# Optimization experiments

Measured on AMD Instinct MI355X. Metric: run time of the kernel, lower is better.

Reference implementation:

```python
import jax, jax.numpy as jnp
import numpy as np

B, M, K, E, V, HOPS = 256, 128, 4, 512, 32000, 3


def setup_inputs() -> dict:
    key = jax.random.key(0)
    ks = jax.random.split(key, 12)

    def emb_table(k):
        t = 0.1 * jax.random.normal(k, (V, E), dtype=jnp.float32)
        return t.at[0].set(0.0)  # padding_idx=0

    inp = {
        "context": jax.random.randint(ks[0], (B, M, K), 0, V),
        "y_": jax.random.randint(ks[1], (B,), 0, V),
        "h_": jax.random.normal(ks[2], (1, B, E), dtype=jnp.float32),
        # embedding tables; C[i] tied to A[i+1], so distinct: A0,A1,A2,C2
        "A0": emb_table(ks[3]),
        "A1": emb_table(ks[4]),
        "A2": emb_table(ks[5]),
        "C2": emb_table(ks[6]),
        # GRU (single layer, single step): PyTorch layout [3E, E] and [3E]
        "W_ih": 0.05 * jax.random.normal(ks[7], (3 * E, E), dtype=jnp.float32),
        "W_hh": 0.05 * jax.random.normal(ks[8], (3 * E, E), dtype=jnp.float32),
        "b_ih": jnp.zeros((3 * E,), dtype=jnp.float32),
        "b_hh": jnp.zeros((3 * E,), dtype=jnp.float32),
        # lin_vocab: Linear(2E -> V)
        "lin_W": 0.02 * jax.random.normal(ks[9], (V, 2 * E), dtype=jnp.float32),
        "lin_b": jnp.zeros((V,), dtype=jnp.float32),
    }
    return inp


def _gru_step(x, h, W_ih, W_hh, b_ih, b_hh):
    gi = x @ W_ih.T + b_ih  # [B, 3E]
    gh = h @ W_hh.T + b_hh
    i_r, i_z, i_n = jnp.split(gi, 3, axis=-1)
    h_r, h_z, h_n = jnp.split(gh, 3, axis=-1)
    r = jax.nn.sigmoid(i_r + h_r)
    z = jax.nn.sigmoid(i_z + h_z)
    n = jnp.tanh(i_n + r * h_n)
    return (1.0 - z) * n + z * h


def reference(context, y_, h_, A0, A1, A2, C2, W_ih, W_hh, b_ih, b_hh, lin_W, lin_b):
    # memories[hop] = sum_k A[hop][context], memories[hops] = sum_k C[hops-1][context]
    tables = [A0, A1, A2, C2]
    memories = [t[context].sum(axis=2) for t in tables]  # each [B, M, E]

    m = A1[y_]  # C[0](y_) -- C[0].weight tied to A[1].weight, [B, E]
    h = _gru_step(m, h_[0], W_ih, W_hh, b_ih, b_hh)  # [B, E]

    q = h
    p = None
    p_vocab = None
    for hop in range(HOPS):
        p = jnp.einsum("bme,be->bm", memories[hop], q)  # dot-attention scores
        attn = jax.nn.softmax(p, axis=1)
        o = jnp.einsum("bm,bme->be", attn, memories[hop + 1])
        if hop == 0:
            p_vocab = jnp.concatenate([q, o], axis=1) @ lin_W.T + lin_b  # [B, V]
        q = q + o

    p_ptr = p  # last hop's pre-softmax scores [B, M]
    return (p_ptr, p_vocab, h[None])  # h: [1, B, E]
```

## Files before the change

### kernel.cpp

```cpp
#include <hip/hip_runtime.h>
#include <hip/hip_bf16.h>
#include <stdint.h>
#include <stddef.h>

#define Bb 256
#define Mm 128
#define Ee 512
#define Vv 32000
#define E3 1536

typedef __attribute__((ext_vector_type(8))) short bf16x8;
typedef __attribute__((ext_vector_type(4))) float f32x4;

__device__ __forceinline__ float bf2f(unsigned short u) {
  union { unsigned int i; float f; } v; v.i = ((unsigned int)u) << 16; return v.f;
}
__device__ __forceinline__ unsigned int f2bf(float f) {
  union { float f; unsigned int u; } v; v.f = f;
  unsigned int u = v.u;
  return ((u + 0x7fffu + ((u >> 16) & 1u)) >> 16);
}

#define IN2F_IDX(bb, col)                                                     \
  ((((size_t)((bb) >> 4) * 32 + ((col) >> 5)) * 512) +                        \
   (size_t)((((bb) & 15) + (((col) >> 3) & 3) * 16) * 8 + ((col) & 7)))

__global__ void convert_kernel(const float* __restrict__ A0, const float* __restrict__ A1,
                               const float* __restrict__ A2,
                               unsigned short* __restrict__ tabB) {
  const int t = blockIdx.y;
  const float* src = (t == 0) ? A0 : (t == 1) ? A1 : A2;
  unsigned short* dst = tabB + (size_t)t * Vv * Ee;
  const int n4 = Vv * Ee / 4;
  for (int i = blockIdx.x * blockDim.x + threadIdx.x; i < n4; i += gridDim.x * blockDim.x) {
    f32x4 v = __builtin_nontemporal_load((const f32x4*)src + i);
    unsigned int o0 = f2bf(v.x) | (f2bf(v.y) << 16);
    unsigned int o1 = f2bf(v.z) | (f2bf(v.w) << 16);
    ((uint2*)dst)[i] = make_uint2(o0, o1);
  }
}

__global__ void gru_gemm_kernel(const int* __restrict__ y,
                                const float* __restrict__ A1,
                                const float* __restrict__ hprev,
                                const float* __restrict__ W_ih,
                                const float* __restrict__ W_hh,
                                float* __restrict__ gi,
                                float* __restrict__ gh) {
  const int z = blockIdx.z;
  const float* W = z ? W_hh : W_ih;
  float* C = z ? gh : gi;
  const int by = blockIdx.x * 64;
  const int jy = blockIdx.y * 64;
  __shared__ float As[16][65];
  __shared__ float Bs[16][65];
  const int tx = threadIdx.x & 15, ty = threadIdx.x >> 4;
  float acc[4][4] = {};
  for (int k0 = 0; k0 < Ee; k0 += 16) {
#pragma unroll
    for (int it = 0; it < 4; ++it) {
      int r = ty + it * 16;
      int row = by + r;
      const float* arow = z ? (hprev + (size_t)row * Ee) : (A1 + (size_t)y[row] * Ee);
      As[tx][r] = arow[k0 + tx];
      Bs[tx][r] = W[(size_t)(jy + r) * Ee + k0 + tx];
    }
    __syncthreads();
#pragma unroll
    for (int kk = 0; kk < 16; ++kk) {
      float a[4], bb[4];
#pragma unroll
      for (int i = 0; i < 4; ++i) { a[i] = As[kk][ty * 4 + i]; bb[i] = Bs[kk][tx * 4 + i]; }
#pragma unroll
      for (int i = 0; i < 4; ++i)
#pragma unroll
        for (int j = 0; j < 4; ++j)
          acc[i][j] += a[i] * bb[j];
    }
    __syncthreads();
  }
#pragma unroll
  for (int i = 0; i < 4; ++i)
#pragma unroll
    for (int j = 0; j < 4; ++j)
      C[(size_t)(by + ty * 4 + i) * E3 + jy + tx * 4 + j] = acc[i][j];
}

__global__ __launch_bounds__(1024) void fused_kernel(
    const int* __restrict__ ctx,
    const unsigned short* __restrict__ tabB,
    const float* __restrict__ A0, const float* __restrict__ A1,
    const float* __restrict__ A2,
    const float* __restrict__ gi, const float* __restrict__ gh,
    const float* __restrict__ b_ih, const float* __restrict__ b_hh,
    const float* __restrict__ h0,
    float* __restrict__ out_h, unsigned short* __restrict__ in2f,
    float* __restrict__ p_out) {
  extern __shared__ char smem[];
  unsigned short* Vlds = (unsigned short*)smem;
  float* p_lds = (float*)(smem + 131072);
  float* qbuf = (float*)(smem + 131584);
  float* obuf = (float*)(smem + 133632);

  const int b = blockIdx.x;
  const int tid = threadIdx.x;
  const int lane = tid & 63, w = tid >> 6;

  if (tid < 512) {
    const int e = tid;
    const float* gib = gi + (size_t)b * E3;
    const float* ghb = gh + (size_t)b * E3;
    float ir = gib[e] + b_ih[e];
    float iz = gib[512 + e] + b_ih[512 + e];
    float inn = gib[1024 + e] + b_ih[1024 + e];
    float hr = ghb[e] + b_hh[e];
    float hz = ghb[512 + e] + b_hh[512 + e];
    float hn = ghb[1024 + e] + b_hh[1024 + e];
    float r = 1.f / (1.f + __expf(-(ir + hr)));
    float z = 1.f / (1.f + __expf(-(iz + hz)));
    float n = tanhf(inn + r * hn);
    float hp = h0[(size_t)b * Ee + e];
    float hnew = (1.f - z) * n + z * hp;
    out_h[(size_t)b * Ee + e] = hnew;
    in2f[IN2F_IDX(b, e)] = (unsigned short)f2bf(hnew);
    qbuf[e] = hnew;
  }

#define GATHER_B(T)                                                          \
  {                                                                          \
    const unsigned short* Tb = tabB + (size_t)(T) * ((size_t)Vv * Ee);       \
    _Pragma("unroll 2")                                                      \
    for (int r8 = 0; r8 < 8; ++r8) {                                         \
      const int row = w * 8 + r8;                                            \
      const int4 cc = *(const int4*)(ctx + ((size_t)b * Mm + row) * 4);      \
      uint4 va = *(const uint4*)(Tb + (size_t)cc.x * Ee + lane * 8);         \
      uint4 vb = *(const uint4*)(Tb + (size_t)cc.y * Ee + lane * 8);         \
      uint4 vc = *(const uint4*)(Tb + (size_t)cc.z * Ee + lane * 8);         \
      uint4 vd = *(const uint4*)(Tb + (size_t)cc.w * Ee + lane * 8);         \
      const unsigned int* pa = (const unsigned int*)&va;                     \
      const unsigned int* pb = (const unsigned int*)&vb;                     \
      const unsigned int* pc = (const unsigned int*)&vc;                     \
      const unsigned int* pd = (const unsigned int*)&vd;                     \
      unsigned int o[4];                                                     \
      _Pragma("unroll")                                                      \
      for (int j = 0; j < 4; ++j) {                                          \
        float lo = bf2f((unsigned short)(pa[j] & 0xffff)) +                  \
                   bf2f((unsigned short)(pb[j] & 0xffff)) +                  \
                   bf2f((unsigned short)(pc[j] & 0xffff)) +                  \
                   bf2f((unsigned short)(pd[j] & 0xffff));                   \
        float hi = bf2f((unsigned short)(pa[j] >> 16)) +                     \
                   bf2f((unsigned short)(pb[j] >> 16)) +                     \
                   bf2f((unsigned short)(pc[j] >> 16)) +                     \
                   bf2f((unsigned short)(pd[j] >> 16));                      \
        o[j] = f2bf(lo) | (f2bf(hi) << 16);                                  \
      }                                                                      \
      *(uint4*)(Vlds + (size_t)row * Ee + lane * 8) = *(uint4*)o;            \
    }                                                                        \
  }

#define GATHER_F(TAB)                                                        \
  {                                                                          \
    _Pragma("unroll 2")                                                      \
    for (int r8 = 0; r8 < 8; ++r8) {                                         \
      const int row = w * 8 + r8;                                            \
      const int4 cc = *(const int4*)(ctx + ((size_t)b * Mm + row) * 4);      \
      const float* s0 = TAB + (size_t)cc.x * Ee + lane * 8;                  \
      const float* s1 = TAB + (size_t)cc.y * Ee + lane * 8;                  \
      const float* s2 = TAB + (size_t)cc.z * Ee + lane * 8;                  \
      const float* s3 = TAB + (size_t)cc.w * Ee + lane * 8;                  \
      float4 a0 = *(const float4*)s0, a1 = *(const float4*)(s0 + 4);         \
      float4 b0 = *(const float4*)s1, b1 = *(const float4*)(s1 + 4);         \
      float4 c0 = *(const float4*)s2, c1 = *(const float4*)(s2 + 4);         \
      float4 d0 = *(const float4*)s3, d1 = *(const float4*)(s3 + 4);         \
      unsigned int o[4];                                                     \
      o[0] = f2bf(a0.x + b0.x + c0.x + d0.x) |                               \
             (f2bf(a0.y + b0.y + c0.y + d0.y) << 16);                        \
      o[1] = f2bf(a0.z + b0.z + c0.z + d0.z) |                               \
             (f2bf(a0.w + b0.w + c0.w + d0.w) << 16);                        \
      o[2] = f2bf(a1.x + b1.x + c1.x + d1.x) |                               \
             (f2bf(a1.y + b1.y + c1.y + d1.y) << 16);                        \
      o[3] = f2bf(a1.z + b1.z + c1.z + d1.z) |                               \
             (f2bf(a1.w + b1.w + c1.w + d1.w) << 16);                        \
      *(uint4*)(Vlds + (size_t)row * Ee + lane * 8) = *(uint4*)o;            \
    }                                                                        \
  }

#define GATHER(T, TAB) { if (tabB) GATHER_B(T) else GATHER_F(TAB) }

#define SCORE_PHASE(EMIT)                                                    \
  {                                                                          \
    float qf[8];                                                             \
    *(float4*)&qf[0] = *(const float4*)&qbuf[lane * 8];                      \
    *(float4*)&qf[4] = *(const float4*)&qbuf[lane * 8 + 4];                  \
    _Pragma("unroll")                                                        \
    for (int r = 0; r < 8; ++r) {                                            \
      const int m = w * 8 + r;                                               \
      uint4 kv = *(const uint4*)(Vlds + (size_t)m * Ee + lane * 8);          \
      const unsigned int* p4 = (const unsigned int*)&kv;                     \
      float s = 0.f;                                                         \
      _Pragma("unroll")                                                      \
      for (int x = 0; x < 4; ++x) {                                          \
        s += bf2f((unsigned short)(p4[x] & 0xffff)) * qf[2 * x];             \
        s += bf2f((unsigned short)(p4[x] >> 16)) * qf[2 * x + 1];            \
      }                                                                      \
      _Pragma("unroll")                                                      \
      for (int off = 32; off > 0; off >>= 1) s += __shfl_down(s, off);       \
      if (lane == 0) { EMIT; }                                               \
    }                                                                        \
  }

#define SOFTMAX_PHASE                                                        \
  if (tid < 64) {                                                            \
    float v0 = p_lds[tid], v1 = p_lds[tid + 64];                             \
    float mx = fmaxf(v0, v1);                                                \
    _Pragma("unroll")                                                        \
    for (int off = 32; off > 0; off >>= 1) mx = fmaxf(mx, __shfl_xor(mx, off)); \
    float e0 = __expf(v0 - mx), e1 = __expf(v1 - mx);                        \
    float s = e0 + e1;                                                       \
    _Pragma("unroll")                                                        \
    for (int off = 32; off > 0; off >>= 1) s += __shfl_xor(s, off);          \
    float inv = 1.f / s;                                                     \
    p_lds[tid] = e0 * inv;                                                   \
    p_lds[tid + 64] = e1 * inv;                                              \
  }

#define O_PHASE                                                              \
  {                                                                          \
    const int g = tid >> 8, t = tid & 255;                                   \
    const int e2 = t * 2;                                                    \
    float a0 = 0.f, a1 = 0.f;                                                \
    _Pragma("unroll 4")                                                      \
    for (int m = g * 32; m < g * 32 + 32; ++m) {                             \
      unsigned int vv = *(const unsigned int*)(Vlds + (size_t)m * Ee + e2);  \
      float ww = p_lds[m];                                                   \
      a0 += ww * bf2f((unsigned short)(vv & 0xffff));                        \
      a1 += ww * bf2f((unsigned short)(vv >> 16));                           \
    }                                                                        \
    obuf[g * 512 + e2] = a0;                                                 \
    obuf[g * 512 + e2 + 1] = a1;                                             \
  }

  GATHER(0, A0)
  __syncthreads();
  SCORE_PHASE(p_lds[m] = s)
  __syncthreads();
  SOFTMAX_PHASE
  GATHER(1, A1)
  __syncthreads();
  O_PHASE
  __syncthreads();
  if (tid < 512) {
    const int e = tid;
    float o = obuf[e] + obuf[512 + e] + obuf[1024 + e] + obuf[1536 + e];
    qbuf[e] = qbuf[e] + o;
    in2f[IN2F_IDX(b, 512 + e)] = (unsigned short)f2bf(o);
  }
  __syncthreads();

  SCORE_PHASE(p_lds[m] = s)
  __syncthreads();
  SOFTMAX_PHASE
  GATHER(2, A2)
  __syncthreads();
  O_PHASE
  __syncthreads();
  if (tid < 512) {
    const int e = tid;
    qbuf[e] = qbuf[e] + obuf[e] + obuf[512 + e] + obuf[1024 + e] + obuf[1536 + e];
  }
  __syncthreads();

  SCORE_PHASE(p_out[b * Mm + m] = s)
}

__global__ __launch_bounds__(512) void pvocab_kernel(
    const unsigned short* __restrict__ in2f,
    const float* __restrict__ lin_W,
    const float* __restrict__ lin_b,
    float* __restrict__ out_pv) {
  const int m0 = blockIdx.x * 128;
  const int v0 = blockIdx.y * 128;
  const int tid = threadIdx.x;
  const int lane = tid & 63, w = tid >> 6;
  const int wm = w >> 2, wn = w & 3;
  const int l15 = lane & 15, lg = lane >> 4;
  __shared__ __align__(16) unsigned short Ws[2][128][64];

  const int wc = tid & 15, wrb = tid >> 4;

  f32x4 acc[4][2];
#pragma unroll
  for (int i = 0; i < 4; ++i)
#pragma unroll
    for (int j = 0; j < 2; ++j)
      acc[i][j] = (f32x4){0.f, 0.f, 0.f, 0.f};

  float4 wR[4];

#define PV_STAGE_LOAD(K0)                                                    \
  {                                                                          \
    _Pragma("unroll")                                                        \
    for (int it = 0; it < 4; ++it) {                                         \
      int r = wrb + it * 32;                                                 \
      wR[it] = *(const float4*)(lin_W + (size_t)(v0 + r) * 1024 + (K0) + wc * 4); \
    }                                                                        \
  }

#define PV_STAGE_WRITE(BUF)                                                  \
  {                                                                          \
    _Pragma("unroll")                                                        \
    for (int it = 0; it < 4; ++it) {                                         \
      int r = wrb + it * 32;                                                 \
      unsigned int o0 = f2bf(wR[it].x) | (f2bf(wR[it].y) << 16);             \
      unsigned int o1 = f2bf(wR[it].z) | (f2bf(wR[it].w) << 16);             \
      int u = wc >> 1, h = wc & 1;                                           \
      *(uint2*)(&Ws[BUF][r][((u + r) & 7) * 8 + h * 4]) = make_uint2(o0, o1); \
    }                                                                        \
  }

  PV_STAGE_LOAD(0)
  PV_STAGE_WRITE(0)
  __syncthreads();

  int cur = 0;
  for (int t = 0; t < 16; ++t) {
    if (t + 1 < 16) PV_STAGE_LOAD((t + 1) * 64)
#pragma unroll
    for (int kk = 0; kk < 2; ++kk) {
      const int cu = kk * 4 + lg;
      const int kb = t * 2 + kk;
      bf16x8 wf[2], af[4];
#pragma unroll
      for (int j = 0; j < 2; ++j) {
        int row = wn * 32 + j * 16 + l15;
        wf[j] = *(const bf16x8*)(&Ws[cur][row][((cu + row) & 7) * 8]);
      }
#pragma unroll
      for (int i = 0; i < 4; ++i) {
        int mblk = (m0 >> 4) + wm * 4 + i;
        af[i] = *(const bf16x8*)(in2f + ((size_t)(mblk * 32 + kb)) * 512 + lane * 8);
      }
#pragma unroll
      for (int i = 0; i < 4; ++i)
#pragma unroll
        for (int j = 0; j < 2; ++j)
          acc[i][j] = __builtin_amdgcn_mfma_f32_16x16x32_bf16(af[i], wf[j], acc[i][j], 0, 0, 0);
    }
    if (t + 1 < 16) {
      PV_STAGE_WRITE(cur ^ 1)
      __syncthreads();
      cur ^= 1;
    }
  }

#pragma unroll
  for (int j = 0; j < 2; ++j) {
    int v = v0 + wn * 32 + j * 16 + l15;
    float bias = lin_b[v];
#pragma unroll
    for (int i = 0; i < 4; ++i) {
      int brow = m0 + wm * 64 + i * 16 + lg * 4;
#pragma unroll
      for (int rr = 0; rr < 4; ++rr)
        out_pv[(size_t)(brow + rr) * Vv + v] = acc[i][j][rr] + bias;
    }
  }
}

extern "C" void kernel_launch(void* const* d_in, const int* in_sizes, int n_in,
                              void* d_out, int out_size, void* d_ws, size_t ws_size,
                              hipStream_t stream) {
  const int* ctx = (const int*)d_in[0];
  const int* y = (const int*)d_in[1];
  const float* h0 = (const float*)d_in[2];
  const float* A0 = (const float*)d_in[3];
  const float* A1 = (const float*)d_in[4];
  const float* A2 = (const float*)d_in[5];
  const float* W_ih = (const float*)d_in[7];
  const float* W_hh = (const float*)d_in[8];
  const float* b_ih = (const float*)d_in[9];
  const float* b_hh = (const float*)d_in[10];
  const float* lin_W = (const float*)d_in[11];
  const float* lin_b = (const float*)d_in[12];

  const size_t tabBytes = (size_t)3 * Vv * Ee * 2;
  const size_t giBytes = (size_t)Bb * E3 * 4;
  const size_t in2Bytes = (size_t)Bb * 1024 * 2;
  const bool bf16path = ws_size >= tabBytes + 2 * giBytes + in2Bytes;

  char* ws = (char*)d_ws;
  size_t off = 0;
  unsigned short* tabB = nullptr;
  if (bf16path) { tabB = (unsigned short*)ws; off += tabBytes; }
  float* gi = (float*)(ws + off); off += giBytes;
  float* gh = (float*)(ws + off); off += giBytes;
  unsigned short* in2f = (unsigned short*)(ws + off);

  float* out = (float*)d_out;
  float* p_ptr = out;
  float* p_voc = out + Bb * Mm;
  float* out_h = out + Bb * Mm + (size_t)Bb * Vv;

  if (bf16path)
    convert_kernel<<<dim3(4096, 3), 256, 0, stream>>>(A0, A1, A2, tabB);
  gru_gemm_kernel<<<dim3(4, 24, 2), 256, 0, stream>>>(y, A1, h0, W_ih, W_hh, gi, gh);
  hipFuncSetAttribute((const void*)fused_kernel,
                      hipFuncAttributeMaxDynamicSharedMemorySize, 141824);
  fused_kernel<<<Bb, 1024, 141824, stream>>>(ctx, tabB, A0, A1, A2, gi, gh,
                                             b_ih, b_hh, h0, out_h, in2f, p_ptr);
  pvocab_kernel<<<dim3(2, Vv / 128), 512, 0, stream>>>(in2f, lin_W, lin_b, p_voc);
}
```

Measured before the change: 228.5 us.

## Retile vocab GEMM to cover all rows per block and merge prep kernels

The vocab projection kernel now gives each block a 64-column vocab slice across all 256 batch rows, instead of a 128x128 tile. Each lin_W row is therefore loaded and converted to bf16 once rather than twice, which cuts the dominant HBM traffic of that GEMM. The table conversion and the GRU gate GEMM are merged into a single launch, with blocks dispatched by block index, to remove one kernel launch. In exchange there are fewer vocab blocks (500) and more MFMA accumulators per wave. The non-bf16 fallback now launches 192 blocks that all take the conversion branch, so that path no longer computes the GRU gates.

```diff
diff --git a/kernel.cpp b/kernel.cpp
--- a/kernel.cpp
+++ b/kernel.cpp
@@ -25,42 +25,45 @@
   ((((size_t)((bb) >> 4) * 32 + ((col) >> 5)) * 512) +                        \
    (size_t)((((bb) & 15) + (((col) >> 3) & 3) * 16) * 8 + ((col) & 7)))
 
-__global__ void convert_kernel(const float* __restrict__ A0, const float* __restrict__ A1,
-                               const float* __restrict__ A2,
-                               unsigned short* __restrict__ tabB) {
-  const int t = blockIdx.y;
-  const float* src = (t == 0) ? A0 : (t == 1) ? A1 : A2;
-  unsigned short* dst = tabB + (size_t)t * Vv * Ee;
-  const int n4 = Vv * Ee / 4;
-  for (int i = blockIdx.x * blockDim.x + threadIdx.x; i < n4; i += gridDim.x * blockDim.x) {
-    f32x4 v = __builtin_nontemporal_load((const f32x4*)src + i);
-    unsigned int o0 = f2bf(v.x) | (f2bf(v.y) << 16);
-    unsigned int o1 = f2bf(v.z) | (f2bf(v.w) << 16);
-    ((uint2*)dst)[i] = make_uint2(o0, o1);
-  }
-}
-
-__global__ void gru_gemm_kernel(const int* __restrict__ y,
-                                const float* __restrict__ A1,
-                                const float* __restrict__ hprev,
-                                const float* __restrict__ W_ih,
-                                const float* __restrict__ W_hh,
-                                float* __restrict__ gi,
-                                float* __restrict__ gh) {
-  const int z = blockIdx.z;
+__global__ void prep_kernel(const float* __restrict__ A0, const float* __restrict__ A1,
+                            const float* __restrict__ A2,
+                            unsigned short* __restrict__ tabB,
+                            const int* __restrict__ y,
+                            const float* __restrict__ hprev,
+                            const float* __restrict__ W_ih,
+                            const float* __restrict__ W_hh,
+                            float* __restrict__ gi,
+                            float* __restrict__ gh) {
+  __shared__ float As[16][65];
+  __shared__ float Bs[16][65];
+  const int bid = blockIdx.x;
+  if (bid < 12288) {
+    const int t = bid >> 12;
+    const int c = bid & 4095;
+    const float* src = (t == 0) ? A0 : (t == 1) ? A1 : A2;
+    unsigned short* dst = tabB + (size_t)t * Vv * Ee;
+    const int n4 = Vv * Ee / 4;
+    for (int i = c * 256 + threadIdx.x; i < n4; i += 4096 * 256) {
+      f32x4 v = __builtin_nontemporal_load((const f32x4*)src + i);
+      unsigned int o0 = f2bf(v.x) | (f2bf(v.y) << 16);
+      unsigned int o1 = f2bf(v.z) | (f2bf(v.w) << 16);
+      ((uint2*)dst)[i] = make_uint2(o0, o1);
+    }
+    return;
+  }
+  const int g = bid - 12288;
+  const int bx = g & 3, by = (g >> 2) % 24, z = g / 96;
   const float* W = z ? W_hh : W_ih;
   float* C = z ? gh : gi;
-  const int by = blockIdx.x * 64;
-  const int jy = blockIdx.y * 64;
-  __shared__ float As[16][65];
-  __shared__ float Bs[16][65];
+  const int byr = bx * 64;
+  const int jy = by * 64;
   const int tx = threadIdx.x & 15, ty = threadIdx.x >> 4;
   float acc[4][4] = {};
   for (int k0 = 0; k0 < Ee; k0 += 16) {
 #pragma unroll
     for (int it = 0; it < 4; ++it) {
       int r = ty + it * 16;
-      int row = by + r;
+      int row = byr + r;
       const float* arow = z ? (hprev + (size_t)row * Ee) : (A1 + (size_t)y[row] * Ee);
       As[tx][r] = arow[k0 + tx];
       Bs[tx][r] = W[(size_t)(jy + r) * Ee + k0 + tx];
@@ -83,7 +86,7 @@
   for (int i = 0; i < 4; ++i)
 #pragma unroll
     for (int j = 0; j < 4; ++j)
-      C[(size_t)(by + ty * 4 + i) * E3 + jy + tx * 4 + j] = acc[i][j];
+      C[(size_t)(byr + ty * 4 + i) * E3 + jy + tx * 4 + j] = acc[i][j];
 }
 
 __global__ __launch_bounds__(1024) void fused_kernel(
@@ -278,29 +281,25 @@
     const float* __restrict__ lin_W,
     const float* __restrict__ lin_b,
     float* __restrict__ out_pv) {
-  const int m0 = blockIdx.x * 128;
-  const int v0 = blockIdx.y * 128;
+  const int v0 = blockIdx.x * 64;
   const int tid = threadIdx.x;
   const int lane = tid & 63, w = tid >> 6;
   const int wm = w >> 2, wn = w & 3;
   const int l15 = lane & 15, lg = lane >> 4;
-  __shared__ __align__(16) unsigned short Ws[2][128][64];
+  __shared__ __align__(16) unsigned short Ws[2][64][64];
 
   const int wc = tid & 15, wrb = tid >> 4;
 
-  f32x4 acc[4][2];
-#pragma unroll
-  for (int i = 0; i < 4; ++i)
-#pragma unroll
-    for (int j = 0; j < 2; ++j)
-      acc[i][j] = (f32x4){0.f, 0.f, 0.f, 0.f};
-
-  float4 wR[4];
+  f32x4 acc[8];
+#pragma unroll
+  for (int i = 0; i < 8; ++i) acc[i] = (f32x4){0.f, 0.f, 0.f, 0.f};
+
+  float4 wR[2];
 
 #define PV_STAGE_LOAD(K0)                                                    \
   {                                                                          \
     _Pragma("unroll")                                                        \
-    for (int it = 0; it < 4; ++it) {                                         \
+    for (int it = 0; it < 2; ++it) {                                         \
       int r = wrb + it * 32;                                                 \
       wR[it] = *(const float4*)(lin_W + (size_t)(v0 + r) * 1024 + (K0) + wc * 4); \
     }                                                                        \
@@ -309,7 +308,7 @@
 #define PV_STAGE_WRITE(BUF)                                                  \
   {                                                                          \
     _Pragma("unroll")                                                        \
-    for (int it = 0; it < 4; ++it) {                                         \
+    for (int it = 0; it < 2; ++it) {                                         \
       int r = wrb + it * 32;                                                 \
       unsigned int o0 = f2bf(wR[it].x) | (f2bf(wR[it].y) << 16);             \
       unsigned int o1 = f2bf(wR[it].z) | (f2bf(wR[it].w) << 16);             \
@@ -329,22 +328,19 @@
     for (int kk = 0; kk < 2; ++kk) {
       const int cu = kk * 4 + lg;
       const int kb = t * 2 + kk;
-      bf16x8 wf[2], af[4];
-#pragma unroll
-      for (int j = 0; j < 2; ++j) {
-        int row = wn * 32 + j * 16 + l15;
-        wf[j] = *(const bf16x8*)(&Ws[cur][row][((cu + row) & 7) * 8]);
+      bf16x8 wf, af[8];
+      {
+        int row = wn * 16 + l15;
+        wf = *(const bf16x8*)(&Ws[cur][row][((cu + row) & 7) * 8]);
       }
 #pragma unroll
-      for (int i = 0; i < 4; ++i) {
-        int mblk = (m0 >> 4) + wm * 4 + i;
+      for (int i = 0; i < 8; ++i) {
+        int mblk = wm * 8 + i;
         af[i] = *(const bf16x8*)(in2f + ((size_t)(mblk * 32 + kb)) * 512 + lane * 8);
       }
 #pragma unroll
-      for (int i = 0; i < 4; ++i)
-#pragma unroll
-        for (int j = 0; j < 2; ++j)
-          acc[i][j] = __builtin_amdgcn_mfma_f32_16x16x32_bf16(af[i], wf[j], acc[i][j], 0, 0, 0);
+      for (int i = 0; i < 8; ++i)
+        acc[i] = __builtin_amdgcn_mfma_f32_16x16x32_bf16(af[i], wf, acc[i], 0, 0, 0);
     }
     if (t + 1 < 16) {
       PV_STAGE_WRITE(cur ^ 1)
@@ -353,16 +349,15 @@
     }
   }
 
-#pragma unroll
-  for (int j = 0; j < 2; ++j) {
-    int v = v0 + wn * 32 + j * 16 + l15;
+  {
+    int v = v0 + wn * 16 + l15;
     float bias = lin_b[v];
 #pragma unroll
-    for (int i = 0; i < 4; ++i) {
-      int brow = m0 + wm * 64 + i * 16 + lg * 4;
+    for (int i = 0; i < 8; ++i) {
+      int brow = wm * 128 + i * 16 + lg * 4;
 #pragma unroll
       for (int rr = 0; rr < 4; ++rr)
-        out_pv[(size_t)(brow + rr) * Vv + v] = acc[i][j][rr] + bias;
+        out_pv[(size_t)(brow + rr) * Vv + v] = acc[i][rr] + bias;
     }
   }
 }
@@ -401,12 +396,14 @@
   float* p_voc = out + Bb * Mm;
   float* out_h = out + Bb * Mm + (size_t)Bb * Vv;
 
-  if (bf16path)
-    convert_kernel<<<dim3(4096, 3), 256, 0, stream>>>(A0, A1, A2, tabB);
-  gru_gemm_kernel<<<dim3(4, 24, 2), 256, 0, stream>>>(y, A1, h0, W_ih, W_hh, gi, gh);
+  if (bf16path) {
+    prep_kernel<<<12480, 256, 0, stream>>>(A0, A1, A2, tabB, y, h0, W_ih, W_hh, gi, gh);
+  } else {
+    prep_kernel<<<dim3(192), 256, 0, stream>>>(A0, A1, A2, tabB, y, h0, W_ih, W_hh, gi, gh);
+  }
   hipFuncSetAttribute((const void*)fused_kernel,
                       hipFuncAttributeMaxDynamicSharedMemorySize, 141824);
   fused_kernel<<<Bb, 1024, 141824, stream>>>(ctx, tabB, A0, A1, A2, gi, gh,
                                              b_ih, b_hh, h0, out_h, in2f, p_ptr);
-  pvocab_kernel<<<dim3(2, Vv / 128), 512, 0, stream>>>(in2f, lin_W, lin_b, p_voc);
-}
+  pvocab_kernel<<<Vv / 64, 512, 0, stream>>>(in2f, lin_W, lin_b, p_voc);
+}
```

After: 260.3 us. +13.9%, slower.
